# Kernel optimization log

Measured on AMD Instinct MI355X. Metric: run time of the kernel, lower is better.

## Reference

```python
import jax, jax.numpy as jnp
import numpy as np

NUM_QUBITS = 22
N_LAYERS = 2
DIM = 2 ** NUM_QUBITS

# CNOT with convention: first index = control, second = target
CNOT = jnp.array([[1, 0, 0, 0],
                  [0, 1, 0, 0],
                  [0, 0, 0, 1],
                  [0, 0, 1, 0]], dtype=jnp.complex64)


def _gate_list():
    """Static circuit spec: per layer, RY on every qubit then a CNOT ladder."""
    gates, p = [], 0
    for _ in range(N_LAYERS):
        for q in range(NUM_QUBITS):
            gates.append(("ry", q, p))
            p += 1
        for q in range(NUM_QUBITS - 1):
            gates.append(("cnot", q, q + 1))
    return gates, p


def _apply_1q(state, U, q):
    # state: (2,)*n complex; contract qubit axis q with 2x2 unitary
    state = jnp.tensordot(U, state, axes=([1], [q]))
    return jnp.moveaxis(state, 0, q)


def _apply_2q(state, U, q0, q1):
    # U: 4x4 unitary acting on qubits (q0, q1)
    state = jnp.tensordot(U.reshape(2, 2, 2, 2), state, axes=([2, 3], [q0, q1]))
    return jnp.moveaxis(state, (0, 1), (q0, q1))


def setup_inputs() -> dict:
    key = jax.random.key(0)
    ks = jax.random.split(key, 9)
    _, n_params = _gate_list()
    return {
        "alpha": jax.random.uniform(ks[0], (3,), jnp.float32),
        "init_alpha_weight": jnp.ones((1,), jnp.float32),
        "w1": jax.random.normal(ks[1], (3, 3), jnp.float32) * 0.5,
        "b1": jax.random.normal(ks[2], (3,), jnp.float32) * 0.1,
        "w2": jax.random.normal(ks[3], (3, 3), jnp.float32) * 0.5,
        "b2": jax.random.normal(ks[4], (3,), jnp.float32) * 0.1,
        "w3": jax.random.normal(ks[5], (2 * DIM, 3), jnp.float32) * 0.02,
        "b3": jax.random.normal(ks[6], (2 * DIM,), jnp.float32) * 0.02,
        "circuit_param": jax.random.uniform(ks[7], (n_params,), jnp.float32) * np.float32(2 * np.pi),
    }


def reference(alpha, init_alpha_weight, w1, b1, w2, b2, w3, b3, circuit_param):
    iaw = init_alpha_weight[0]
    # tiny residual MLP (torch Linear: W @ x + b for a vector input)
    y = jnp.tanh(w1 @ alpha + b1) + alpha * iaw
    a = y
    y = jnp.tanh(w2 @ y + b2) + a * iaw
    y = w3 @ y + b3                      # (2 * 2^n,)
    real, imag = y[:DIM], y[DIM:]
    norm = jnp.sqrt(jnp.sum(real * real + imag * imag))
    state = jax.lax.complex(real / norm, imag / norm).reshape((2,) * NUM_QUBITS)
    # gate-by-gate statevector simulation
    gates, _ = _gate_list()
    zeros22 = jnp.zeros((2, 2), jnp.float32)
    for g in gates:
        if g[0] == "ry":
            th = circuit_param[g[2]] * 0.5
            c, s = jnp.cos(th), jnp.sin(th)
            U = jax.lax.complex(jnp.stack([jnp.stack([c, -s]), jnp.stack([s, c])]), zeros22)
            state = _apply_1q(state, U, g[1])
        else:  # cnot
            state = _apply_2q(state, CNOT, g[1], g[2])
    amps = state.reshape(-1)
    return amps.real ** 2 + amps.imag ** 2  # measurement probabilities, (2^n,) float32
```

## Files before the change

### kernel.cpp

```cpp
#include <hip/hip_runtime.h>

#define DIM 4194304

__device__ __forceinline__ int pfx(int x) {
  x ^= x >> 1; x ^= x >> 2; x ^= x >> 4; x ^= x >> 8;
  return x;
}

__global__ void k0_prep(const float* __restrict__ alpha, const float* __restrict__ iawp,
                        const float* __restrict__ w1, const float* __restrict__ b1,
                        const float* __restrict__ w2, const float* __restrict__ b2,
                        const float* __restrict__ cp,
                        float* __restrict__ cs, double* __restrict__ sumsq,
                        float* __restrict__ yout, double* __restrict__ partial) {
  int t = threadIdx.x;
  partial[t] = 0.0;
  if (t < 44) {
    int L = t / 22, b = t % 22;
    int q = 21 - b;
    float th = cp[L * 22 + q] * 0.5f;
    cs[2 * t]     = cosf(th);
    cs[2 * t + 1] = sinf(th);
  }
  if (t == 0) {
    *sumsq = 0.0;
    float iaw = iawp[0];
    float a[3] = {alpha[0], alpha[1], alpha[2]};
    float y[3], z[3];
    for (int i = 0; i < 3; ++i)
      y[i] = tanhf(w1[i*3]*a[0] + w1[i*3+1]*a[1] + w1[i*3+2]*a[2] + b1[i]) + a[i]*iaw;
    for (int i = 0; i < 3; ++i)
      z[i] = tanhf(w2[i*3]*y[0] + w2[i*3+1]*y[1] + w2[i*3+2]*y[2] + b2[i]) + y[i]*iaw;
    yout[0] = z[0]; yout[1] = z[1]; yout[2] = z[2];
  }
}

__global__ __launch_bounds__(1024) void k1_init_lo(
    const float* __restrict__ w3, const float* __restrict__ b3,
    const float* __restrict__ y3, float* __restrict__ A,
    double* __restrict__ partial, const float* __restrict__ cs) {
  __shared__ float lds[16384];
  const int tid = threadIdx.x;
  const int i_base = blockIdx.x << 14;
  const float y0 = y3[0], y1 = y3[1], y2 = y3[2];
  const float c0 = cs[0], s0 = cs[1], c1 = cs[2], s1 = cs[3];
  float acc = 0.f;
  for (int r = 0; r < 4; ++r) {
    int j = (r * 1024 + tid) * 4;
    int e = i_base + j;
    const float4* wp = (const float4*)(w3 + (long)e * 3);
    float4 wa = wp[0], wb = wp[1], wc = wp[2];
    float4 bb = *(const float4*)(b3 + e);
    float4 amp;
    amp.x = wa.x*y0 + wa.y*y1 + wa.z*y2 + bb.x;
    amp.y = wa.w*y0 + wb.x*y1 + wb.y*y2 + bb.y;
    amp.z = wb.z*y0 + wb.w*y1 + wc.x*y2 + bb.z;
    amp.w = wc.y*y0 + wc.z*y1 + wc.w*y2 + bb.w;
    acc += amp.x*amp.x + amp.y*amp.y + amp.z*amp.z + amp.w*amp.w;
    { float a0 = amp.x, a1 = amp.y; amp.x = c0*a0 - s0*a1; amp.y = s0*a0 + c0*a1; }
    { float a0 = amp.z, a1 = amp.w; amp.z = c0*a0 - s0*a1; amp.w = s0*a0 + c0*a1; }
    { float a0 = amp.x, a1 = amp.z; amp.x = c1*a0 - s1*a1; amp.z = s1*a0 + c1*a1; }
    { float a0 = amp.y, a1 = amp.w; amp.y = c1*a0 - s1*a1; amp.w = s1*a0 + c1*a1; }
    *(float4*)(lds + j) = amp;
  }
  double d = (double)acc;
  for (int o = 32; o > 0; o >>= 1) d += __shfl_down(d, o, 64);
  if ((tid & 63) == 0) atomicAdd(&partial[blockIdx.x], d);
#pragma unroll
  for (int t = 2; t < 14; ++t) {
    float c = cs[t * 2], s = cs[t * 2 + 1];
    __syncthreads();
    for (int pi = 0; pi < 8; ++pi) {
      int i  = pi * 1024 + tid;
      int i0 = ((i >> t) << (t + 1)) | (i & ((1 << t) - 1));
      int i1 = i0 | (1 << t);
      float a0 = lds[i0], a1 = lds[i1];
      lds[i0] = c * a0 - s * a1;
      lds[i1] = s * a0 + c * a1;
    }
  }
  __syncthreads();
  for (int r = 0; r < 4; ++r) {
    int j = (r * 1024 + tid) * 4;
    *(float4*)(A + i_base + j) = *(float4*)(lds + j);
  }
}

__global__ __launch_bounds__(1024) void k2_hi(float* __restrict__ A,
                                              const float* __restrict__ cs,
                                              const double* __restrict__ partial,
                                              double* __restrict__ sumsq) {
  __shared__ float lds[16384];
  const int tid = threadIdx.x;
  if (blockIdx.x == 0 && tid < 512) {
    double d = partial[tid];
    for (int o = 32; o > 0; o >>= 1) d += __shfl_down(d, o, 64);
    if ((tid & 63) == 0) atomicAdd(sumsq, d);
  }
  const int plane = blockIdx.x >> 8;
  const int w8 = blockIdx.x & 255;
  float* base = A + plane * DIM + w8 * 32;
  for (int r = 0; r < 4; ++r) {
    int idx = r * 1024 + tid;
    int h = idx >> 4, b13 = (idx >> 3) & 1, q = idx & 7;
    *(float4*)(lds + h * 64 + b13 * 32 + q * 4) =
        *(const float4*)(base + h * 16384 + b13 * 8192 + q * 4);
  }
#pragma unroll
  for (int tb = 0; tb < 8; ++tb) {
    float c = cs[(14 + tb) * 2], s = cs[(14 + tb) * 2 + 1];
    __syncthreads();
    for (int pi = 0; pi < 8; ++pi) {
      int i = pi * 1024 + tid;
      int col = i & 63, ph = i >> 6;
      int h0 = ((ph >> tb) << (tb + 1)) | (ph & ((1 << tb) - 1));
      int h1 = h0 | (1 << tb);
      float a0 = lds[h0 * 64 + col], a1 = lds[h1 * 64 + col];
      lds[h0 * 64 + col] = c * a0 - s * a1;
      lds[h1 * 64 + col] = s * a0 + c * a1;
    }
  }
  {
    float c = cs[(22 + 14) * 2], s = cs[(22 + 14) * 2 + 1];
    __syncthreads();
    for (int pi = 0; pi < 8; ++pi) {
      int i = pi * 1024 + tid;
      int col = i & 63;
      int he = (i >> 6) << 1;
      int par = __popc(he) & 1;
      int iA = he * 64 + col, iB = (he ^ 1) * 64 + (col ^ 32);
      int i0 = par ? iB : iA, i1 = par ? iA : iB;
      float a0 = lds[i0], a1 = lds[i1];
      lds[i0] = c * a0 - s * a1;
      lds[i1] = s * a0 + c * a1;
    }
  }
#pragma unroll
  for (int b = 15; b <= 21; ++b) {
    float c = cs[(22 + b) * 2], s = cs[(22 + b) * 2 + 1];
    const int sh = b - 14;
    const int mR = 3 << (sh - 1);
    __syncthreads();
    for (int pi = 0; pi < 8; ++pi) {
      int i = pi * 1024 + tid;
      int col = i & 63, ph = i >> 6;
      int h0 = ((ph >> sh) << (sh + 1)) | (ph & ((1 << sh) - 1));
      int h1 = h0 ^ mR;
      int par = __popc(h0 >> (sh + 1)) & 1;
      int i0 = (par ? h1 : h0) * 64 + col;
      int i1 = (par ? h0 : h1) * 64 + col;
      float a0 = lds[i0], a1 = lds[i1];
      lds[i0] = c * a0 - s * a1;
      lds[i1] = s * a0 + c * a1;
    }
  }
  __syncthreads();
  for (int r = 0; r < 4; ++r) {
    int idx = r * 1024 + tid;
    int h = idx >> 4, b13 = (idx >> 3) & 1, q = idx & 7;
    *(float4*)(base + h * 16384 + b13 * 8192 + q * 4) =
        *(float4*)(lds + h * 64 + b13 * 32 + q * 4);
  }
}

__global__ __launch_bounds__(1024) void k3_perm_lo(float* __restrict__ A,
                                                   const float* __restrict__ cs) {
  __shared__ float lds[16384];
  const int tid = threadIdx.x;
  const int plane = blockIdx.x >> 8;
  const int H = blockIdx.x & 255;
  const int c8 = H ^ (H >> 1);
  const int flip = (H & 1) << 13;
  float* base = A + plane * DIM + (c8 << 14);
  for (int r = 0; r < 4; ++r) {
    int j = (r * 1024 + tid) * 4;
    *(float4*)(lds + j) = *(const float4*)(base + j);
  }
#pragma unroll
  for (int t = 0; t < 14; ++t) {
    float c = cs[(22 + t) * 2], s = cs[(22 + t) * 2 + 1];
    __syncthreads();
    for (int pi = 0; pi < 8; ++pi) {
      int i  = pi * 1024 + tid;
      int l0 = ((i >> t) << (t + 1)) | (i & ((1 << t) - 1));
      int l1 = l0 | (1 << t);
      int p0 = (l0 ^ (l0 >> 1)) ^ flip;
      int p1 = (l1 ^ (l1 >> 1)) ^ flip;
      float a0 = lds[p0], a1 = lds[p1];
      lds[p0] = c * a0 - s * a1;
      lds[p1] = s * a0 + c * a1;
    }
  }
  __syncthreads();
  for (int r = 0; r < 4; ++r) {
    int j = (r * 1024 + tid) * 4;
    *(float4*)(base + j) = *(float4*)(lds + j);
  }
}

__global__ __launch_bounds__(256) void k4_prob(const float* __restrict__ A,
                                               float* __restrict__ out,
                                               const double* __restrict__ sumsq) {
  const float inv = (float)(1.0 / *sumsq);
  int g = blockIdx.x * 256 + threadIdx.x;
  int j4 = g << 2;
  int pos = j4 ^ (j4 >> 2);
  int pb = pos & ~3, sh = pos & 3;
  float4 re = *(const float4*)(A + pb);
  float4 im = *(const float4*)(A + DIM + pb);
  if (sh & 1) {
    float t;
    t = re.x; re.x = re.y; re.y = t;  t = re.z; re.z = re.w; re.w = t;
    t = im.x; im.x = im.y; im.y = t;  t = im.z; im.z = im.w; im.w = t;
  }
  if (sh & 2) {
    float t;
    t = re.x; re.x = re.z; re.z = t;  t = re.y; re.y = re.w; re.w = t;
    t = im.x; im.x = im.z; im.z = t;  t = im.y; im.y = im.w; im.w = t;
  }
  float4 o;
  o.x = (re.x*re.x + im.x*im.x) * inv;
  o.y = (re.y*re.y + im.y*im.y) * inv;
  o.z = (re.z*re.z + im.z*im.z) * inv;
  o.w = (re.w*re.w + im.w*im.w) * inv;
  *(float4*)(out + j4) = o;
}

extern "C" void kernel_launch(void* const* d_in, const int* in_sizes, int n_in,
                              void* d_out, int out_size, void* d_ws, size_t ws_size,
                              hipStream_t stream) {
  const float* alpha = (const float*)d_in[0];
  const float* iaw   = (const float*)d_in[1];
  const float* w1    = (const float*)d_in[2];
  const float* b1    = (const float*)d_in[3];
  const float* w2    = (const float*)d_in[4];
  const float* b2    = (const float*)d_in[5];
  const float* w3    = (const float*)d_in[6];
  const float* b3    = (const float*)d_in[7];
  const float* cp    = (const float*)d_in[8];
  float* outp = (float*)d_out;

  char* w = (char*)d_ws;
  double* sumsq   = (double*)w;
  float*  cs      = (float*)(w + 64);
  float*  yv      = (float*)(w + 512);
  double* partial = (double*)(w + 1024);
  float*  A       = (float*)(w + 8192);

  k0_prep<<<1, 512, 0, stream>>>(alpha, iaw, w1, b1, w2, b2, cp, cs, sumsq, yv, partial);
  k1_init_lo<<<512, 1024, 0, stream>>>(w3, b3, yv, A, partial, cs);
  k2_hi<<<512, 1024, 0, stream>>>(A, cs, partial, sumsq);
  k3_perm_lo<<<512, 1024, 0, stream>>>(A, cs);
  k4_prob<<<4096, 256, 0, stream>>>(A, outp, sumsq);
}
```

Baseline: 286.7 us.

## Fuse qubit rotations into radix-4 float4 register passes with fewer LDS syncs

Restructures the three statevector kernels so each LDS pass applies two rotation gates at once on float4 vectors held in registers (radix-4 butterflies). Some gates are applied entirely in registers before or after the shared-memory stage. The CNOT ladder is handled through parity-dependent sign flips in a conjugated frame instead of explicit Gray-code permuted indexing. This roughly halves the number of barriers and scalar LDS round trips per kernel. The cost is intricate index and sign logic that is easy to get wrong, plus higher register pressure under the new launch bounds.

```diff
diff --git a/kernel.cpp b/kernel.cpp
--- a/kernel.cpp
+++ b/kernel.cpp
@@ -2,10 +2,30 @@
 
 #define DIM 4194304
 
-__device__ __forceinline__ int pfx(int x) {
-  x ^= x >> 1; x ^= x >> 2; x ^= x >> 4; x ^= x >> 8;
-  return x;
-}
+__device__ __forceinline__ void bfs(float4& X, float4& Y, float c, float ss) {
+  float4 t = X;
+  X.x = c*t.x + ss*Y.x; X.y = c*t.y + ss*Y.y;
+  X.z = c*t.z + ss*Y.z; X.w = c*t.w + ss*Y.w;
+  Y.x = c*Y.x - ss*t.x; Y.y = c*Y.y - ss*t.y;
+  Y.z = c*Y.z - ss*t.z; Y.w = c*Y.w - ss*t.w;
+}
+__device__ __forceinline__ void bfs_sw2(float4& X, float4& Y, float c, float ss) {
+  float4 t = X;
+  X.x = c*t.x + ss*Y.z; X.y = c*t.y + ss*Y.w;
+  X.z = c*t.z + ss*Y.x; X.w = c*t.w + ss*Y.y;
+  Y.x = c*Y.x - ss*t.z; Y.y = c*Y.y - ss*t.w;
+  Y.z = c*Y.z - ss*t.x; Y.w = c*Y.w - ss*t.y;
+}
+
+#define PASS4(QB, A1, A2, C1, SS1, C2, SS2)                           \
+  { __syncthreads();                                                  \
+    int _q = (QB);                                                    \
+    float4 F0 = L4[_q], F1 = L4[_q^(A1)], F2 = L4[_q^(A2)],           \
+           F3 = L4[_q^(A1)^(A2)];                                     \
+    bfs(F0, F1, (C1), (SS1)); bfs(F2, F3, (C1), (SS1));               \
+    bfs(F0, F2, (C2), (SS2)); bfs(F1, F3, (C2), (SS2));               \
+    L4[_q] = F0; L4[_q^(A1)] = F1; L4[_q^(A2)] = F2;                  \
+    L4[_q^(A1)^(A2)] = F3; }
 
 __global__ void k0_prep(const float* __restrict__ alpha, const float* __restrict__ iawp,
                         const float* __restrict__ w1, const float* __restrict__ b1,
@@ -35,20 +55,20 @@
   }
 }
 
-__global__ __launch_bounds__(1024) void k1_init_lo(
+__global__ __launch_bounds__(1024, 8) void k1_init_lo(
     const float* __restrict__ w3, const float* __restrict__ b3,
     const float* __restrict__ y3, float* __restrict__ A,
     double* __restrict__ partial, const float* __restrict__ cs) {
   __shared__ float lds[16384];
+  float4* L4 = (float4*)lds;
   const int tid = threadIdx.x;
-  const int i_base = blockIdx.x << 14;
+  const long i_base = (long)blockIdx.x << 14;
   const float y0 = y3[0], y1 = y3[1], y2 = y3[2];
-  const float c0 = cs[0], s0 = cs[1], c1 = cs[2], s1 = cs[3];
+  float4 f[4];
   float acc = 0.f;
   for (int r = 0; r < 4; ++r) {
-    int j = (r * 1024 + tid) * 4;
-    int e = i_base + j;
-    const float4* wp = (const float4*)(w3 + (long)e * 3);
+    long e = i_base + r * 4096 + tid * 4;
+    const float4* wp = (const float4*)(w3 + e * 3);
     float4 wa = wp[0], wb = wp[1], wc = wp[2];
     float4 bb = *(const float4*)(b3 + e);
     float4 amp;
@@ -57,40 +77,47 @@
     amp.z = wb.z*y0 + wb.w*y1 + wc.x*y2 + bb.z;
     amp.w = wc.y*y0 + wc.z*y1 + wc.w*y2 + bb.w;
     acc += amp.x*amp.x + amp.y*amp.y + amp.z*amp.z + amp.w*amp.w;
-    { float a0 = amp.x, a1 = amp.y; amp.x = c0*a0 - s0*a1; amp.y = s0*a0 + c0*a1; }
-    { float a0 = amp.z, a1 = amp.w; amp.z = c0*a0 - s0*a1; amp.w = s0*a0 + c0*a1; }
-    { float a0 = amp.x, a1 = amp.z; amp.x = c1*a0 - s1*a1; amp.z = s1*a0 + c1*a1; }
-    { float a0 = amp.y, a1 = amp.w; amp.y = c1*a0 - s1*a1; amp.w = s1*a0 + c1*a1; }
-    *(float4*)(lds + j) = amp;
-  }
+    f[r] = amp;
+  }
+  {
+    const float c0 = cs[0], s0 = cs[1], c1 = cs[2], s1 = cs[3];
+    for (int r = 0; r < 4; ++r) {
+      float4 a = f[r];
+      float nx = c0*a.x - s0*a.y, ny = c0*a.y + s0*a.x;
+      float nz = c0*a.z - s0*a.w, nw = c0*a.w + s0*a.z;
+      a.x = c1*nx - s1*nz; a.z = c1*nz + s1*nx;
+      a.y = c1*ny - s1*nw; a.w = c1*nw + s1*ny;
+      f[r] = a;
+    }
+    const float cA = cs[24], sA = cs[25], cB = cs[26], sB = cs[27];
+    bfs(f[0], f[1], cA, -sA); bfs(f[2], f[3], cA, -sA);
+    bfs(f[0], f[2], cB, -sB); bfs(f[1], f[3], cB, -sB);
+  }
+  for (int r = 0; r < 4; ++r) L4[r * 1024 + tid] = f[r];
   double d = (double)acc;
   for (int o = 32; o > 0; o >>= 1) d += __shfl_down(d, o, 64);
   if ((tid & 63) == 0) atomicAdd(&partial[blockIdx.x], d);
-#pragma unroll
-  for (int t = 2; t < 14; ++t) {
-    float c = cs[t * 2], s = cs[t * 2 + 1];
-    __syncthreads();
-    for (int pi = 0; pi < 8; ++pi) {
-      int i  = pi * 1024 + tid;
-      int i0 = ((i >> t) << (t + 1)) | (i & ((1 << t) - 1));
-      int i1 = i0 | (1 << t);
-      float a0 = lds[i0], a1 = lds[i1];
-      lds[i0] = c * a0 - s * a1;
-      lds[i1] = s * a0 + c * a1;
-    }
-  }
+  PASS4(tid * 4,                      1,     2,     cs[4],  -cs[5],  cs[6],  -cs[7]);
+  PASS4((tid&3)   | ((tid>>2) << 4),  4,     8,     cs[8],  -cs[9],  cs[10], -cs[11]);
+  PASS4((tid&15)  | ((tid>>4) << 6),  0x10,  0x20,  cs[12], -cs[13], cs[14], -cs[15]);
+  PASS4((tid&63)  | ((tid>>6) << 8),  0x40,  0x80,  cs[16], -cs[17], cs[18], -cs[19]);
   __syncthreads();
-  for (int r = 0; r < 4; ++r) {
-    int j = (r * 1024 + tid) * 4;
-    *(float4*)(A + i_base + j) = *(float4*)(lds + j);
-  }
-}
-
-__global__ __launch_bounds__(1024) void k2_hi(float* __restrict__ A,
-                                              const float* __restrict__ cs,
-                                              const double* __restrict__ partial,
-                                              double* __restrict__ sumsq) {
+  {
+    int q = (tid & 255) | ((tid >> 8) << 10);
+    float4 F0 = L4[q], F1 = L4[q^0x100], F2 = L4[q^0x200], F3 = L4[q^0x300];
+    bfs(F0, F1, cs[20], -cs[21]); bfs(F2, F3, cs[20], -cs[21]);
+    bfs(F0, F2, cs[22], -cs[23]); bfs(F1, F3, cs[22], -cs[23]);
+    float4* A4 = (float4*)A + (i_base >> 2);
+    A4[q] = F0; A4[q^0x100] = F1; A4[q^0x200] = F2; A4[q^0x300] = F3;
+  }
+}
+
+__global__ __launch_bounds__(1024, 8) void k2_hi(float* __restrict__ A,
+                                                 const float* __restrict__ cs,
+                                                 const double* __restrict__ partial,
+                                                 double* __restrict__ sumsq) {
   __shared__ float lds[16384];
+  float4* L4 = (float4*)lds;
   const int tid = threadIdx.x;
   if (blockIdx.x == 0 && tid < 512) {
     double d = partial[tid];
@@ -99,102 +126,122 @@
   }
   const int plane = blockIdx.x >> 8;
   const int w8 = blockIdx.x & 255;
-  float* base = A + plane * DIM + w8 * 32;
+  float4* B4 = (float4*)(A + plane * DIM + w8 * 32);
   for (int r = 0; r < 4; ++r) {
     int idx = r * 1024 + tid;
     int h = idx >> 4, b13 = (idx >> 3) & 1, q = idx & 7;
-    *(float4*)(lds + h * 64 + b13 * 32 + q * 4) =
-        *(const float4*)(base + h * 16384 + b13 * 8192 + q * 4);
-  }
-#pragma unroll
-  for (int tb = 0; tb < 8; ++tb) {
-    float c = cs[(14 + tb) * 2], s = cs[(14 + tb) * 2 + 1];
-    __syncthreads();
-    for (int pi = 0; pi < 8; ++pi) {
-      int i = pi * 1024 + tid;
-      int col = i & 63, ph = i >> 6;
-      int h0 = ((ph >> tb) << (tb + 1)) | (ph & ((1 << tb) - 1));
-      int h1 = h0 | (1 << tb);
-      float a0 = lds[h0 * 64 + col], a1 = lds[h1 * 64 + col];
-      lds[h0 * 64 + col] = c * a0 - s * a1;
-      lds[h1 * 64 + col] = s * a0 + c * a1;
-    }
-  }
-  {
-    float c = cs[(22 + 14) * 2], s = cs[(22 + 14) * 2 + 1];
-    __syncthreads();
-    for (int pi = 0; pi < 8; ++pi) {
-      int i = pi * 1024 + tid;
-      int col = i & 63;
-      int he = (i >> 6) << 1;
-      int par = __popc(he) & 1;
-      int iA = he * 64 + col, iB = (he ^ 1) * 64 + (col ^ 32);
-      int i0 = par ? iB : iA, i1 = par ? iA : iB;
-      float a0 = lds[i0], a1 = lds[i1];
-      lds[i0] = c * a0 - s * a1;
-      lds[i1] = s * a0 + c * a1;
-    }
-  }
-#pragma unroll
-  for (int b = 15; b <= 21; ++b) {
-    float c = cs[(22 + b) * 2], s = cs[(22 + b) * 2 + 1];
-    const int sh = b - 14;
-    const int mR = 3 << (sh - 1);
-    __syncthreads();
-    for (int pi = 0; pi < 8; ++pi) {
-      int i = pi * 1024 + tid;
-      int col = i & 63, ph = i >> 6;
-      int h0 = ((ph >> sh) << (sh + 1)) | (ph & ((1 << sh) - 1));
-      int h1 = h0 ^ mR;
-      int par = __popc(h0 >> (sh + 1)) & 1;
-      int i0 = (par ? h1 : h0) * 64 + col;
-      int i1 = (par ? h0 : h1) * 64 + col;
-      float a0 = lds[i0], a1 = lds[i1];
-      lds[i0] = c * a0 - s * a1;
-      lds[i1] = s * a0 + c * a1;
-    }
+    L4[(h << 4) | (b13 << 3) | q] = B4[h * 4096 + b13 * 2048 + q];
+  }
+  PASS4((tid&15)  | ((tid>>4) << 6),  0x10,  0x20,  cs[28], -cs[29], cs[30], -cs[31]);
+  PASS4((tid&63)  | ((tid>>6) << 8),  0x40,  0x80,  cs[32], -cs[33], cs[34], -cs[35]);
+  PASS4((tid&255) | ((tid>>8) << 10), 0x100, 0x200, cs[36], -cs[37], cs[38], -cs[39]);
+  PASS4(tid,                          0x400, 0x800, cs[40], -cs[41], cs[42], -cs[43]);
+  { int hi = tid >> 1;
+    int q = (hi & 7) | ((tid & 1) << 3) | ((hi >> 3) << 6);
+    float s1 = (__popc(q >> 4) & 1) ? cs[73] : -cs[73];
+    float s2 = (__popc(q >> 5) & 1) ? cs[75] : -cs[75];
+    PASS4(q, 0x18, 0x30, cs[72], s1, cs[74], s2);
+  }
+  { int hi = tid >> 1;
+    int q = (hi & 0x1F) | ((tid & 1) << 5) | ((hi >> 5) << 8);
+    float s1 = (__popc(q >> 6) & 1) ? cs[77] : -cs[77];
+    float s2 = (__popc(q >> 7) & 1) ? cs[79] : -cs[79];
+    PASS4(q, 0x60, 0xC0, cs[76], s1, cs[78], s2);
+  }
+  { int hi = tid >> 1;
+    int q = (hi & 0x7F) | ((tid & 1) << 7) | ((hi >> 7) << 10);
+    float s1 = (__popc(q >> 8) & 1) ? cs[81] : -cs[81];
+    float s2 = (__popc(q >> 9) & 1) ? cs[83] : -cs[83];
+    PASS4(q, 0x180, 0x300, cs[80], s1, cs[82], s2);
+  }
+  { int hi = tid >> 1;
+    int q = (hi & 0x1FF) | ((tid & 1) << 9);
+    float s1 = (__popc(q >> 10) & 1) ? cs[85] : -cs[85];
+    float s2 = (__popc(q >> 11) & 1) ? cs[87] : -cs[87];
+    PASS4(q, 0x600, 0xC00, cs[84], s1, cs[86], s2);
   }
   __syncthreads();
   for (int r = 0; r < 4; ++r) {
     int idx = r * 1024 + tid;
     int h = idx >> 4, b13 = (idx >> 3) & 1, q = idx & 7;
-    *(float4*)(base + h * 16384 + b13 * 8192 + q * 4) =
-        *(float4*)(lds + h * 64 + b13 * 32 + q * 4);
-  }
-}
-
-__global__ __launch_bounds__(1024) void k3_perm_lo(float* __restrict__ A,
-                                                   const float* __restrict__ cs) {
+    B4[h * 4096 + b13 * 2048 + q] = L4[(h << 4) | (b13 << 3) | q];
+  }
+}
+
+__global__ __launch_bounds__(1024, 8) void k3_conj_lo(float* __restrict__ A,
+                                                      const float* __restrict__ cs) {
   __shared__ float lds[16384];
+  float4* L4 = (float4*)lds;
   const int tid = threadIdx.x;
   const int plane = blockIdx.x >> 8;
-  const int H = blockIdx.x & 255;
-  const int c8 = H ^ (H >> 1);
-  const int flip = (H & 1) << 13;
-  float* base = A + plane * DIM + (c8 << 14);
-  for (int r = 0; r < 4; ++r) {
-    int j = (r * 1024 + tid) * 4;
-    *(float4*)(lds + j) = *(const float4*)(base + j);
-  }
-#pragma unroll
-  for (int t = 0; t < 14; ++t) {
-    float c = cs[(22 + t) * 2], s = cs[(22 + t) * 2 + 1];
-    __syncthreads();
-    for (int pi = 0; pi < 8; ++pi) {
-      int i  = pi * 1024 + tid;
-      int l0 = ((i >> t) << (t + 1)) | (i & ((1 << t) - 1));
-      int l1 = l0 | (1 << t);
-      int p0 = (l0 ^ (l0 >> 1)) ^ flip;
-      int p1 = (l1 ^ (l1 >> 1)) ^ flip;
-      float a0 = lds[p0], a1 = lds[p1];
-      lds[p0] = c * a0 - s * a1;
-      lds[p1] = s * a0 + c * a1;
+  const int c8 = blockIdx.x & 255;
+  const int Pc = __popc(c8) & 1;
+  float4* A4 = (float4*)A + (((long)plane * DIM + ((long)c8 << 14)) >> 2);
+  float4 f[4];
+  for (int r = 0; r < 4; ++r) f[r] = A4[r * 1024 + tid];
+  const int T = (__popc(tid) & 1) ^ Pc;
+  {
+    const float c0 = cs[44], s0 = cs[45], c1v = cs[46], s1v = cs[47];
+    for (int r = 0; r < 4; ++r) {
+      int rho = ((r ^ (r >> 1)) & 1) ^ T;
+      float ss0 = rho ? s0 : -s0;
+      float ss1 = rho ? s1v : -s1v;
+      float4 a = f[r];
+      float nx = c0*a.x + ss0*a.y, ny = c0*a.y - ss0*a.x;
+      float nz = c0*a.z - ss0*a.w, nw = c0*a.w + ss0*a.z;
+      a.x = c1v*nx + ss1*nw; a.w = c1v*nw - ss1*nx;
+      a.y = c1v*ny + ss1*nz; a.z = c1v*nz - ss1*ny;
+      f[r] = a;
     }
-  }
+    const float cD = cs[70], sD = cs[71];
+    float ssD = Pc ? sD : -sD;
+    bfs(f[0], f[3], cD, ssD); bfs(f[1], f[2], cD, ssD);
+  }
+  for (int r = 0; r < 4; ++r) L4[r * 1024 + tid] = f[r];
   __syncthreads();
-  for (int r = 0; r < 4; ++r) {
-    int j = (r * 1024 + tid) * 4;
-    *(float4*)(base + j) = *(float4*)(lds + j);
+  {
+    int q = tid * 4;
+    float4 F0 = L4[q], F1 = L4[q^1], F2 = L4[q^2], F3 = L4[q^3];
+    const float c2v = cs[48], s2v = cs[49], c3v = cs[50], s3v = cs[51];
+    float ss2 = T ? s2v : -s2v;
+    bfs_sw2(F0, F1, c2v, ss2); bfs_sw2(F2, F3, c2v, -ss2);
+    float ss3 = T ? s3v : -s3v;
+    bfs(F0, F3, c3v, ss3); bfs(F1, F2, c3v, ss3);
+    L4[q] = F0; L4[q^1] = F1; L4[q^2] = F2; L4[q^3] = F3;
+  }
+  { int hi = tid >> 1;
+    int q = (hi & 1) | ((tid & 1) << 3) | ((hi >> 1) << 4);
+    float s1 = ((__popc(q >> 2) & 1) ^ Pc) ? cs[53] : -cs[53];
+    float s2 = ((__popc(q >> 3) & 1) ^ Pc) ? cs[55] : -cs[55];
+    PASS4(q, 6, 0xC, cs[52], s1, cs[54], s2);
+  }
+  { int hi = tid >> 1;
+    int q = (hi & 7) | ((tid & 1) << 3) | ((hi >> 3) << 6);
+    float s1 = ((__popc(q >> 4) & 1) ^ Pc) ? cs[57] : -cs[57];
+    float s2 = ((__popc(q >> 5) & 1) ^ Pc) ? cs[59] : -cs[59];
+    PASS4(q, 0x18, 0x30, cs[56], s1, cs[58], s2);
+  }
+  { int hi = tid >> 1;
+    int q = (hi & 0x1F) | ((tid & 1) << 5) | ((hi >> 5) << 8);
+    float s1 = ((__popc(q >> 6) & 1) ^ Pc) ? cs[61] : -cs[61];
+    float s2 = ((__popc(q >> 7) & 1) ^ Pc) ? cs[63] : -cs[63];
+    PASS4(q, 0x60, 0xC0, cs[60], s1, cs[62], s2);
+  }
+  { int hi = tid >> 1;
+    int q = (hi & 0x7F) | ((tid & 1) << 7) | ((hi >> 7) << 10);
+    float s1 = ((__popc(q >> 8) & 1) ^ Pc) ? cs[65] : -cs[65];
+    float s2 = ((__popc(q >> 9) & 1) ^ Pc) ? cs[67] : -cs[67];
+    PASS4(q, 0x180, 0x300, cs[64], s1, cs[66], s2);
+  }
+  __syncthreads();
+  {
+    const float cE = cs[68], sE = cs[69];
+    float ssE = Pc ? sE : -sE;
+    int qa = tid, qb = tid | 0x800;
+    float4 F0 = L4[qa], F1 = L4[qa^0x600], F2 = L4[qb], F3 = L4[qb^0x600];
+    bfs(F0, F1, cE, ssE);
+    bfs(F2, F3, cE, -ssE);
+    A4[qa] = F0; A4[qa^0x600] = F1; A4[qb] = F2; A4[qb^0x600] = F3;
   }
 }
 
@@ -250,6 +297,6 @@
   k0_prep<<<1, 512, 0, stream>>>(alpha, iaw, w1, b1, w2, b2, cp, cs, sumsq, yv, partial);
   k1_init_lo<<<512, 1024, 0, stream>>>(w3, b3, yv, A, partial, cs);
   k2_hi<<<512, 1024, 0, stream>>>(A, cs, partial, sumsq);
-  k3_perm_lo<<<512, 1024, 0, stream>>>(A, cs);
+  k3_conj_lo<<<512, 1024, 0, stream>>>(A, cs);
   k4_prob<<<4096, 256, 0, stream>>>(A, outp, sumsq);
 }
```

Result: faster. 246.4 us (-14.0%).
